# Optimization experiments

Measured on AMD Instinct MI355X. Metric: run time of the kernel, lower is better.

## Reference

```python
import jax, jax.numpy as jnp
import numpy as np

N_NODES = 50000
EPS = 1e-5


def _gcn_edges(edge_index, num_nodes):
    # Add self loops (PyG GCNConv default) and compute symmetric normalization.
    src = jnp.concatenate([edge_index[0], jnp.arange(num_nodes, dtype=edge_index.dtype)])
    dst = jnp.concatenate([edge_index[1], jnp.arange(num_nodes, dtype=edge_index.dtype)])
    deg = jax.ops.segment_sum(jnp.ones_like(dst, dtype=jnp.float32), dst, num_segments=num_nodes)
    dinv = jnp.where(deg > 0, jax.lax.rsqrt(deg), 0.0)
    norm = dinv[src] * dinv[dst]  # [E+N]
    return src, dst, norm


def gcn_conv(x, W, b, src, dst, norm, num_nodes):
    xw = x @ W  # [N, out]
    msg = xw[src] * norm[:, None]  # [E+N, out] gather + scale
    out = jax.ops.segment_sum(msg, dst, num_segments=num_nodes)  # scatter-add
    return out + b


def layer_norm(x, g, b):
    mu = jnp.mean(x, axis=-1, keepdims=True)
    var = jnp.mean(jnp.square(x - mu), axis=-1, keepdims=True)
    return (x - mu) * jax.lax.rsqrt(var + EPS) * g + b


def setup_inputs() -> dict:
    key = jax.random.key(0)
    ks = jax.random.split(key, 12)
    d_in, d_h, d_out = 128, 128, 64
    n_edges = 800000
    x = jax.random.normal(ks[0], (N_NODES, d_in), dtype=jnp.float32)
    edge_index = jax.random.randint(ks[1], (2, n_edges), 0, N_NODES, dtype=jnp.int64)
    s = 1.0 / np.sqrt(d_in)
    return {
        "x": x,
        "edge_index": edge_index,
        "W1": jax.random.uniform(ks[2], (d_in, d_h), jnp.float32, -s, s),
        "b1": jnp.zeros((d_h,), jnp.float32),
        "W2": jax.random.uniform(ks[3], (d_h, d_h), jnp.float32, -s, s),
        "b2": jnp.zeros((d_h,), jnp.float32),
        "W3": jax.random.uniform(ks[4], (d_h, d_out), jnp.float32, -s, s),
        "b3": jnp.zeros((d_out,), jnp.float32),
        "g1": jnp.ones((d_h,), jnp.float32),
        "be1": jnp.zeros((d_h,), jnp.float32),
        "g2": jnp.ones((d_h,), jnp.float32),
        "be2": jnp.zeros((d_h,), jnp.float32),
    }


def reference(x, edge_index, W1, b1, W2, b2, W3, b3, g1, be1, g2, be2):
    num_nodes = x.shape[0]
    src, dst, norm = _gcn_edges(edge_index, num_nodes)
    h = jax.nn.relu(gcn_conv(x, W1, b1, src, dst, norm, num_nodes))
    h = layer_norm(h, g1, be1)  # dropout is identity in eval mode
    h = jax.nn.relu(gcn_conv(h, W2, b2, src, dst, norm, num_nodes))
    h = layer_norm(h, g2, be2)
    return gcn_conv(h, W3, b3, src, dst, norm, num_nodes)
```

## Files before the change

### kernel.cpp

```cpp
#include <hip/hip_runtime.h>

#define EPSV 1e-5f

typedef _Float16 half2_t __attribute__((ext_vector_type(2)));
typedef _Float16 half8_t __attribute__((ext_vector_type(8)));
typedef float float4_t __attribute__((ext_vector_type(4)));

#define BINSH 6
#define BINSZ 64


__global__ __launch_bounds__(256) void k_pre(
    const float* __restrict__ W1, const float* __restrict__ W2,
    const float* __restrict__ W3, _Float16* __restrict__ Wh1,
    _Float16* __restrict__ Wh2, _Float16* __restrict__ Wh3,
    int* __restrict__ cursor, _Float16* __restrict__ ys_y,
    _Float16* __restrict__ ys3, int N, int N1, int zb) {
  int bid = blockIdx.x;
  if (bid < 20) {
    const float* W;
    _Float16* Wh;
    int COLS, t;
    if (bid < 8) { W = W1; Wh = Wh1; COLS = 128; t = bid * 256 + threadIdx.x; }
    else if (bid < 16) { W = W2; Wh = Wh2; COLS = 128; t = (bid - 8) * 256 + threadIdx.x; }
    else { W = W3; Wh = Wh3; COLS = 64; t = (bid - 16) * 256 + threadIdx.x; }
    int NT = (COLS / 16) * 4 * 64;
    if (t >= NT) return;
    int lane = t & 63;
    int ks = (t >> 6) & 3;
    int nb = t >> 8;
    int col = nb * 16 + (lane & 15);
    int k0 = ks * 32 + (lane >> 4) * 8;
    half8_t v;
#pragma unroll
    for (int j = 0; j < 8; j++) v[j] = (_Float16)W[(size_t)(k0 + j) * COLS + col];
    *(half8_t*)&Wh[(size_t)t * 8] = v;
    return;
  }
  if (bid < 20 + zb) {
    int i4 = (bid - 20) * 256 + threadIdx.x;
    if (i4 < ((N + 3) >> 2)) ((int4*)cursor)[i4] = make_int4(0, 0, 0, 0);
    return;
  }
  int t = threadIdx.x;
  half8_t z;
#pragma unroll
  for (int j = 0; j < 8; j++) z[j] = (_Float16)0.f;
  if (t < 16) {
    int s = t >> 2, qq = t & 3;
    *(half8_t*)&ys_y[((size_t)s * N1 + N) * 32 + qq * 8] = z;
  } else if (t < 24) {
    int j = t - 16;
    int s = j >> 2, qq = j & 3;
    *(half8_t*)&ys3[((size_t)s * N1 + N) * 32 + qq * 8] = z;
  }
}


__global__ __launch_bounds__(256) void k_init(
    const int* __restrict__ src, const int* __restrict__ dst,
    int* __restrict__ cursor, int* __restrict__ csr, int E, int N) {
  int b = blockIdx.x;
  int slice = b & 7;
  int lo = (int)(((long long)N * slice) >> 3);
  int hi = (int)(((long long)N * (slice + 1)) >> 3);
  int r = (b >> 3) * 256 + threadIdx.x;
  const int stride = (4096 >> 3) * 256;
  int E4 = E >> 2;
  const int4* dst4 = (const int4*)dst;
  const int4* src4 = (const int4*)src;
  for (int e4 = r; e4 < E4; e4 += stride) {
    int4 d4 = dst4[e4];
    int4 s4 = src4[e4];
    if (d4.x >= lo && d4.x < hi) {
      int pos = atomicAdd(&cursor[d4.x], 1);
      if (pos < BINSZ) csr[((size_t)d4.x << BINSH) + pos] = s4.x;
    }
    if (d4.y >= lo && d4.y < hi) {
      int pos = atomicAdd(&cursor[d4.y], 1);
      if (pos < BINSZ) csr[((size_t)d4.y << BINSH) + pos] = s4.y;
    }
    if (d4.z >= lo && d4.z < hi) {
      int pos = atomicAdd(&cursor[d4.z], 1);
      if (pos < BINSZ) csr[((size_t)d4.z << BINSH) + pos] = s4.z;
    }
    if (d4.w >= lo && d4.w < hi) {
      int pos = atomicAdd(&cursor[d4.w], 1);
      if (pos < BINSZ) csr[((size_t)d4.w << BINSH) + pos] = s4.w;
    }
  }
  if ((E & 3) && (b >> 3) == 0) {
    for (int e = (E & ~3) + threadIdx.x; e < E; e += 256) {
      int d = dst[e];
      if (d >= lo && d < hi) {
        int s = src[e];
        int pos = atomicAdd(&cursor[d], 1);
        if (pos < BINSZ) csr[((size_t)d << BINSH) + pos] = s;
      }
    }
  }
}


template <int COLS, bool LN, typename AT>
__device__ __forceinline__ void gemm_body(
    int bx, const AT* __restrict__ A, const float2* __restrict__ lnp,
    const float* __restrict__ g, const float* __restrict__ be,
    const _Float16* __restrict__ Wh, const int* __restrict__ cursor,
    _Float16* __restrict__ out, int N, int N1) {
  constexpr int NB = COLS / 16;
  int lane = threadIdx.x & 63;
  int w = threadIdx.x >> 6;
  int quad = lane >> 4;
  int mrow = bx * 64 + w * 16 + (lane & 15);
  half8_t af[4];
  if (mrow < N) {
    if constexpr (LN) {
      float P = 0.f, Q = 0.f;
#pragma unroll
      for (int s = 0; s < 4; s++) {
        float2 pq = lnp[(size_t)s * N + mrow];
        P += pq.x; Q += pq.y;
      }
      float mean = P * (1.f / 128.f);
      float rstd = rsqrtf(Q * (1.f / 128.f) - mean * mean + EPSV);
#pragma unroll
      for (int ks = 0; ks < 4; ks++) {
        half8_t sv = *(const half8_t*)&A[((size_t)ks * N1 + mrow) * 32 + quad * 8];
        float4 g0 = *(const float4*)&g[ks * 32 + quad * 8];
        float4 g1 = *(const float4*)&g[ks * 32 + quad * 8 + 4];
        float4 e0 = *(const float4*)&be[ks * 32 + quad * 8];
        float4 e1 = *(const float4*)&be[ks * 32 + quad * 8 + 4];
        af[ks][0] = (_Float16)fmaf(((float)sv[0] - mean) * rstd, g0.x, e0.x);
        af[ks][1] = (_Float16)fmaf(((float)sv[1] - mean) * rstd, g0.y, e0.y);
        af[ks][2] = (_Float16)fmaf(((float)sv[2] - mean) * rstd, g0.z, e0.z);
        af[ks][3] = (_Float16)fmaf(((float)sv[3] - mean) * rstd, g0.w, e0.w);
        af[ks][4] = (_Float16)fmaf(((float)sv[4] - mean) * rstd, g1.x, e1.x);
        af[ks][5] = (_Float16)fmaf(((float)sv[5] - mean) * rstd, g1.y, e1.y);
        af[ks][6] = (_Float16)fmaf(((float)sv[6] - mean) * rstd, g1.z, e1.z);
        af[ks][7] = (_Float16)fmaf(((float)sv[7] - mean) * rstd, g1.w, e1.w);
      }
    } else {
      const AT* ap = A + (size_t)mrow * 128 + quad * 8;
#pragma unroll
      for (int ks = 0; ks < 4; ks++) {
        float4 f0 = *(const float4*)(ap + ks * 32);
        float4 f1 = *(const float4*)(ap + ks * 32 + 4);
        af[ks][0] = (_Float16)f0.x; af[ks][1] = (_Float16)f0.y;
        af[ks][2] = (_Float16)f0.z; af[ks][3] = (_Float16)f0.w;
        af[ks][4] = (_Float16)f1.x; af[ks][5] = (_Float16)f1.y;
        af[ks][6] = (_Float16)f1.z; af[ks][7] = (_Float16)f1.w;
      }
    }
  } else {
#pragma unroll
    for (int ks = 0; ks < 4; ks++)
#pragma unroll
      for (int j = 0; j < 8; j++) af[ks][j] = (_Float16)0.f;
  }
  float4_t acc[NB];
#pragma unroll
  for (int nb = 0; nb < NB; nb++) acc[nb] = (float4_t){0.f, 0.f, 0.f, 0.f};
#pragma unroll
  for (int nb = 0; nb < NB; nb++) {
#pragma unroll
    for (int ks = 0; ks < 4; ks++) {
      half8_t bf = *(const half8_t*)&Wh[(size_t)((nb * 4 + ks) * 64 + lane) * 8];
      acc[nb] = __builtin_amdgcn_mfma_f32_16x16x32_f16(af[ks], bf, acc[nb], 0, 0, 0);
    }
  }
  int orow0 = bx * 64 + w * 16 + quad * 4;
#pragma unroll
  for (int r = 0; r < 4; r++) {
    int row = orow0 + r;
    if (row < N) {
      float dv = rsqrtf((float)(min(cursor[row], BINSZ) + 1));
#pragma unroll
      for (int nb = 0; nb < NB; nb++) {
        int dim = nb * 16 + (lane & 15);
        out[((size_t)(dim >> 5) * N1 + row) * 32 + (dim & 31)] =
            (_Float16)(acc[nb][r] * dv);
      }
    }
  }
}

template <int COLS, bool LN, typename AT>
__global__ __launch_bounds__(256) void k_gemm_mfma(
    const AT* __restrict__ A, const float2* __restrict__ lnp,
    const float* __restrict__ g, const float* __restrict__ be,
    const _Float16* __restrict__ Wh, const int* __restrict__ cursor,
    _Float16* __restrict__ out, int N, int N1) {
  gemm_body<COLS, LN, AT>(blockIdx.x, A, lnp, g, be, Wh, cursor, out, N, N1);
}


__global__ __launch_bounds__(256) void k_aggs(
    const _Float16* __restrict__ ysrc, const int* __restrict__ csr,
    const int* __restrict__ cursor, const float* __restrict__ b,
    _Float16* __restrict__ sdst, float2* __restrict__ lnp, int N, int N1) {
  int slice = blockIdx.x & 3;
  int lane = threadIdx.x & 63;
  int g = lane >> 4, li = lane & 15;
  int q = li & 3, es = li >> 2;
  int node = (blockIdx.x >> 2) * 16 + (threadIdx.x >> 6) * 4 + g;
  const half8_t* yb = (const half8_t*)ysrc + (size_t)slice * N1 * 4;
  int cnt = 0;
  if (node < N) cnt = min(cursor[node], BINSZ);
  int cround = (cnt + 15) & ~15;
  size_t bin = (size_t)node << BINSH;
  float acc[8];
#pragma unroll
  for (int j = 0; j < 8; j++) acc[j] = 0.f;
  const half2_t one2 = {(_Float16)1.f, (_Float16)1.f};
  for (int c = 0; c < cround; c += 16) {
    int idx = N;
    if (c + li < cnt) idx = csr[bin + c + li];
#pragma unroll
    for (int p = 0; p < 2; p++) {
      int sa = __shfl(idx, (g << 4) | (es << 2) | (p << 1), 64);
      int sb = __shfl(idx, (g << 4) | (es << 2) | (p << 1) | 1, 64);
      half8_t ua = yb[(size_t)sa * 4 + q];
      half8_t ub = yb[(size_t)sb * 4 + q];
      const unsigned int* wa = (const unsigned int*)&ua;
      const unsigned int* wb = (const unsigned int*)&ub;
#pragma unroll
      for (int w = 0; w < 4; w++) {
        unsigned int p0 = __builtin_amdgcn_perm(wa[w], wb[w], 0x01000504u);
        unsigned int p1 = __builtin_amdgcn_perm(wa[w], wb[w], 0x03020706u);
        acc[2 * w] = __builtin_amdgcn_fdot2(
            __builtin_bit_cast(half2_t, p0), one2, acc[2 * w], false);
        acc[2 * w + 1] = __builtin_amdgcn_fdot2(
            __builtin_bit_cast(half2_t, p1), one2, acc[2 * w + 1], false);
      }
    }
  }
#pragma unroll
  for (int j = 0; j < 8; j++) {
    acc[j] += __shfl_xor(acc[j], 4, 64);
    acc[j] += __shfl_xor(acc[j], 8, 64);
  }
  half8_t us = yb[(size_t)min(node, N) * 4 + q];
#pragma unroll
  for (int j = 0; j < 8; j++) acc[j] += (float)us[j];
  float di = rsqrtf((float)(cnt + 1));
  float4 b0 = ((const float4*)b)[slice * 8 + q * 2];
  float4 b1 = ((const float4*)b)[slice * 8 + q * 2 + 1];
  float v[8];
  v[0] = fmaxf(fmaf(acc[0], di, b0.x), 0.f);
  v[1] = fmaxf(fmaf(acc[1], di, b0.y), 0.f);
  v[2] = fmaxf(fmaf(acc[2], di, b0.z), 0.f);
  v[3] = fmaxf(fmaf(acc[3], di, b0.w), 0.f);
  v[4] = fmaxf(fmaf(acc[4], di, b1.x), 0.f);
  v[5] = fmaxf(fmaf(acc[5], di, b1.y), 0.f);
  v[6] = fmaxf(fmaf(acc[6], di, b1.z), 0.f);
  v[7] = fmaxf(fmaf(acc[7], di, b1.w), 0.f);
  float p = 0.f, qs = 0.f;
#pragma unroll
  for (int j = 0; j < 8; j++) {
    p += v[j];
    qs = fmaf(v[j], v[j], qs);
  }
  p += __shfl_xor(p, 1, 64);
  p += __shfl_xor(p, 2, 64);
  qs += __shfl_xor(qs, 1, 64);
  qs += __shfl_xor(qs, 2, 64);
  if (node < N) {
    if (li == 0) lnp[(size_t)slice * N + node] = make_float2(p, qs);
    if (es == 0) {
      half8_t o;
#pragma unroll
      for (int j = 0; j < 8; j++) o[j] = (_Float16)v[j];
      ((half8_t*)sdst)[((size_t)slice * N1 + node) * 4 + q] = o;
    }
  }
}


__global__ __launch_bounds__(256) void k_agg_out(
    const _Float16* __restrict__ ysrc, const int* __restrict__ csr,
    const int* __restrict__ cursor, const float* __restrict__ b,
    float* __restrict__ out, int N, int N1) {
  int slice = blockIdx.x & 1;
  int lane = threadIdx.x & 63;
  int g = lane >> 4, li = lane & 15;
  int q = li & 3, es = li >> 2;
  int node = (blockIdx.x >> 1) * 16 + (threadIdx.x >> 6) * 4 + g;
  const half8_t* yb = (const half8_t*)ysrc + (size_t)slice * N1 * 4;
  int cnt = 0;
  if (node < N) cnt = min(cursor[node], BINSZ);
  int cround = (cnt + 15) & ~15;
  size_t bin = (size_t)node << BINSH;
  float acc[8];
#pragma unroll
  for (int j = 0; j < 8; j++) acc[j] = 0.f;
  const half2_t one2 = {(_Float16)1.f, (_Float16)1.f};
  for (int c = 0; c < cround; c += 16) {
    int idx = N;
    if (c + li < cnt) idx = csr[bin + c + li];
#pragma unroll
    for (int p = 0; p < 2; p++) {
      int sa = __shfl(idx, (g << 4) | (es << 2) | (p << 1), 64);
      int sb = __shfl(idx, (g << 4) | (es << 2) | (p << 1) | 1, 64);
      half8_t ua = yb[(size_t)sa * 4 + q];
      half8_t ub = yb[(size_t)sb * 4 + q];
      const unsigned int* wa = (const unsigned int*)&ua;
      const unsigned int* wb = (const unsigned int*)&ub;
#pragma unroll
      for (int w = 0; w < 4; w++) {
        unsigned int p0 = __builtin_amdgcn_perm(wa[w], wb[w], 0x01000504u);
        unsigned int p1 = __builtin_amdgcn_perm(wa[w], wb[w], 0x03020706u);
        acc[2 * w] = __builtin_amdgcn_fdot2(
            __builtin_bit_cast(half2_t, p0), one2, acc[2 * w], false);
        acc[2 * w + 1] = __builtin_amdgcn_fdot2(
            __builtin_bit_cast(half2_t, p1), one2, acc[2 * w + 1], false);
      }
    }
  }
#pragma unroll
  for (int j = 0; j < 8; j++) {
    acc[j] += __shfl_xor(acc[j], 4, 64);
    acc[j] += __shfl_xor(acc[j], 8, 64);
  }
  if (node < N && es == 0) {
    half8_t us = yb[(size_t)node * 4 + q];
#pragma unroll
    for (int j = 0; j < 8; j++) acc[j] += (float)us[j];
    float di = rsqrtf((float)(cnt + 1));
    float4 b0 = ((const float4*)b)[slice * 8 + q * 2];
    float4 b1 = ((const float4*)b)[slice * 8 + q * 2 + 1];
    float4 o0, o1;
    o0.x = fmaf(acc[0], di, b0.x);
    o0.y = fmaf(acc[1], di, b0.y);
    o0.z = fmaf(acc[2], di, b0.z);
    o0.w = fmaf(acc[3], di, b0.w);
    o1.x = fmaf(acc[4], di, b1.x);
    o1.y = fmaf(acc[5], di, b1.y);
    o1.z = fmaf(acc[6], di, b1.z);
    o1.w = fmaf(acc[7], di, b1.w);
    ((float4*)out)[(size_t)node * 16 + slice * 8 + q * 2] = o0;
    ((float4*)out)[(size_t)node * 16 + slice * 8 + q * 2 + 1] = o1;
  }
}


extern "C" void kernel_launch(void* const* d_in, const int* in_sizes, int n_in,
                              void* d_out, int out_size, void* d_ws, size_t ws_size,
                              hipStream_t stream) {
  const float* x = (const float*)d_in[0];
  const int* ei = (const int*)d_in[1];
  const float* W1 = (const float*)d_in[2];
  const float* b1 = (const float*)d_in[3];
  const float* W2 = (const float*)d_in[4];
  const float* b2 = (const float*)d_in[5];
  const float* W3 = (const float*)d_in[6];
  const float* b3 = (const float*)d_in[7];
  const float* g1 = (const float*)d_in[8];
  const float* be1 = (const float*)d_in[9];
  const float* g2 = (const float*)d_in[10];
  const float* be2 = (const float*)d_in[11];

  int N = in_sizes[0] / 128;
  int E = in_sizes[1] / 2;
  int N1 = N + 1;
  const int* srcs = ei;
  const int* dsts = ei + E;

  char* ws = (char*)d_ws;
  size_t off = 0;
  auto alloc = [&](size_t bytes) -> char* {
    char* p = ws + off;
    off = (off + bytes + 255) & ~(size_t)255;
    return p;
  };
  int* cursor = (int*)alloc((size_t)N * 4);
  int* csr = (int*)alloc((size_t)N * BINSZ * 4);
  _Float16* ys_y = (_Float16*)alloc((size_t)4 * N1 * 32 * 2);
  _Float16* ys_s = (_Float16*)alloc((size_t)4 * N1 * 32 * 2);
  _Float16* ys3 = (_Float16*)alloc((size_t)2 * N1 * 32 * 2);
  float2* lnp = (float2*)alloc((size_t)4 * N * 8);
  _Float16* Wh1 = (_Float16*)alloc(128 * 128 * 2);
  _Float16* Wh2 = (_Float16*)alloc(128 * 128 * 2);
  _Float16* Wh3 = (_Float16*)alloc(128 * 64 * 2);

  int gb = (N + 63) / 64;
  int nb16 = (N + 15) / 16;
  int zb = (((N + 3) >> 2) + 255) >> 8;

  k_pre<<<20 + zb + 1, 256, 0, stream>>>(W1, W2, W3, Wh1, Wh2, Wh3,
                                         cursor, ys_y, ys3, N, N1, zb);
  k_init<<<4096, 256, 0, stream>>>(srcs, dsts, cursor, csr, E, N);
  k_gemm_mfma<128, false, float><<<gb, 256, 0, stream>>>(
      x, nullptr, nullptr, nullptr, Wh1, cursor, ys_y, N, N1);
  k_aggs<<<nb16 * 4, 256, 0, stream>>>(ys_y, csr, cursor, b1, ys_s, lnp, N, N1);
  k_gemm_mfma<128, true, _Float16><<<gb, 256, 0, stream>>>(
      ys_s, lnp, g1, be1, Wh2, cursor, ys_y, N, N1);
  k_aggs<<<nb16 * 4, 256, 0, stream>>>(ys_y, csr, cursor, b2, ys_s, lnp, N, N1);
  k_gemm_mfma<64, true, _Float16><<<gb, 256, 0, stream>>>(
      ys_s, lnp, g2, be2, Wh3, cursor, ys3, N, N1);
  k_agg_out<<<nb16 * 2, 256, 0, stream>>>(ys3, csr, cursor, b3,
                                          (float*)d_out, N, N1);
}
```

Measured before the change: 244.2 us.

## Fuse first GEMM with CSR fill and apply source degree scaling in aggregation

The first layer's GEMM no longer needs degree counts, so it is merged into the CSR-building kernel as extra blocks and runs concurrently with the atomic binning. Because the GEMM output is now unscaled, the first aggregation kernel applies the per-source rsqrt-degree weight inside the fdot2 and scales the self term by the node's own factor. The cursor array grows by one entry and is zeroed so the padding node index N reads a valid count. This removes one kernel launch and its serialization, at the cost of extra cursor gathers per edge in the first aggregation and fp16 rounding of the weights.

Result: no change. 247.3 us (+1.3%).

```diff
diff --git a/kernel.cpp b/kernel.cpp
--- a/kernel.cpp
+++ b/kernel.cpp
@@ -39,7 +39,7 @@
   }
   if (bid < 20 + zb) {
     int i4 = (bid - 20) * 256 + threadIdx.x;
-    if (i4 < ((N + 3) >> 2)) ((int4*)cursor)[i4] = make_int4(0, 0, 0, 0);
+    if (i4 < ((N1 + 3) >> 2)) ((int4*)cursor)[i4] = make_int4(0, 0, 0, 0);
     return;
   }
   int t = threadIdx.x;
@@ -57,10 +57,111 @@
 }
 
 
-__global__ __launch_bounds__(256) void k_init(
+template <int COLS, bool LN, bool SCALE, typename AT>
+__device__ __forceinline__ void gemm_body(
+    int bx, const AT* __restrict__ A, const float2* __restrict__ lnp,
+    const float* __restrict__ g, const float* __restrict__ be,
+    const _Float16* __restrict__ Wh, const int* __restrict__ cursor,
+    _Float16* __restrict__ out, int N, int N1) {
+  constexpr int NB = COLS / 16;
+  int lane = threadIdx.x & 63;
+  int w = threadIdx.x >> 6;
+  int quad = lane >> 4;
+  int mrow = bx * 64 + w * 16 + (lane & 15);
+  half8_t af[4];
+  if (mrow < N) {
+    if constexpr (LN) {
+      float P = 0.f, Q = 0.f;
+#pragma unroll
+      for (int s = 0; s < 4; s++) {
+        float2 pq = lnp[(size_t)s * N + mrow];
+        P += pq.x; Q += pq.y;
+      }
+      float mean = P * (1.f / 128.f);
+      float rstd = rsqrtf(Q * (1.f / 128.f) - mean * mean + EPSV);
+#pragma unroll
+      for (int ks = 0; ks < 4; ks++) {
+        half8_t sv = *(const half8_t*)&A[((size_t)ks * N1 + mrow) * 32 + quad * 8];
+        float4 g0 = *(const float4*)&g[ks * 32 + quad * 8];
+        float4 g1 = *(const float4*)&g[ks * 32 + quad * 8 + 4];
+        float4 e0 = *(const float4*)&be[ks * 32 + quad * 8];
+        float4 e1 = *(const float4*)&be[ks * 32 + quad * 8 + 4];
+        af[ks][0] = (_Float16)fmaf(((float)sv[0] - mean) * rstd, g0.x, e0.x);
+        af[ks][1] = (_Float16)fmaf(((float)sv[1] - mean) * rstd, g0.y, e0.y);
+        af[ks][2] = (_Float16)fmaf(((float)sv[2] - mean) * rstd, g0.z, e0.z);
+        af[ks][3] = (_Float16)fmaf(((float)sv[3] - mean) * rstd, g0.w, e0.w);
+        af[ks][4] = (_Float16)fmaf(((float)sv[4] - mean) * rstd, g1.x, e1.x);
+        af[ks][5] = (_Float16)fmaf(((float)sv[5] - mean) * rstd, g1.y, e1.y);
+        af[ks][6] = (_Float16)fmaf(((float)sv[6] - mean) * rstd, g1.z, e1.z);
+        af[ks][7] = (_Float16)fmaf(((float)sv[7] - mean) * rstd, g1.w, e1.w);
+      }
+    } else {
+      const AT* ap = A + (size_t)mrow * 128 + quad * 8;
+#pragma unroll
+      for (int ks = 0; ks < 4; ks++) {
+        float4 f0 = *(const float4*)(ap + ks * 32);
+        float4 f1 = *(const float4*)(ap + ks * 32 + 4);
+        af[ks][0] = (_Float16)f0.x; af[ks][1] = (_Float16)f0.y;
+        af[ks][2] = (_Float16)f0.z; af[ks][3] = (_Float16)f0.w;
+        af[ks][4] = (_Float16)f1.x; af[ks][5] = (_Float16)f1.y;
+        af[ks][6] = (_Float16)f1.z; af[ks][7] = (_Float16)f1.w;
+      }
+    }
+  } else {
+#pragma unroll
+    for (int ks = 0; ks < 4; ks++)
+#pragma unroll
+      for (int j = 0; j < 8; j++) af[ks][j] = (_Float16)0.f;
+  }
+  float4_t acc[NB];
+#pragma unroll
+  for (int nb = 0; nb < NB; nb++) acc[nb] = (float4_t){0.f, 0.f, 0.f, 0.f};
+#pragma unroll
+  for (int nb = 0; nb < NB; nb++) {
+#pragma unroll
+    for (int ks = 0; ks < 4; ks++) {
+      half8_t bf = *(const half8_t*)&Wh[(size_t)((nb * 4 + ks) * 64 + lane) * 8];
+      acc[nb] = __builtin_amdgcn_mfma_f32_16x16x32_f16(af[ks], bf, acc[nb], 0, 0, 0);
+    }
+  }
+  int orow0 = bx * 64 + w * 16 + quad * 4;
+#pragma unroll
+  for (int r = 0; r < 4; r++) {
+    int row = orow0 + r;
+    if (row < N) {
+      float dv = 1.f;
+      if constexpr (SCALE) dv = rsqrtf((float)(min(cursor[row], BINSZ) + 1));
+#pragma unroll
+      for (int nb = 0; nb < NB; nb++) {
+        int dim = nb * 16 + (lane & 15);
+        out[((size_t)(dim >> 5) * N1 + row) * 32 + (dim & 31)] =
+            (_Float16)(SCALE ? acc[nb][r] * dv : acc[nb][r]);
+      }
+    }
+  }
+}
+
+template <int COLS, bool LN, bool SCALE, typename AT>
+__global__ __launch_bounds__(256) void k_gemm_mfma(
+    const AT* __restrict__ A, const float2* __restrict__ lnp,
+    const float* __restrict__ g, const float* __restrict__ be,
+    const _Float16* __restrict__ Wh, const int* __restrict__ cursor,
+    _Float16* __restrict__ out, int N, int N1) {
+  gemm_body<COLS, LN, SCALE, AT>(blockIdx.x, A, lnp, g, be, Wh, cursor, out, N, N1);
+}
+
+
+__global__ __launch_bounds__(256) void k_fill_gemm1(
+    const float* __restrict__ x, const _Float16* __restrict__ Wh1,
     const int* __restrict__ src, const int* __restrict__ dst,
-    int* __restrict__ cursor, int* __restrict__ csr, int E, int N) {
-  int b = blockIdx.x;
+    int* __restrict__ cursor, int* __restrict__ csr,
+    _Float16* __restrict__ ys_y, int E, int N, int N1, int gb) {
+  if ((int)blockIdx.x < gb) {
+    gemm_body<128, false, false, float>(blockIdx.x, x, nullptr, nullptr,
+                                        nullptr, Wh1, nullptr, ys_y, N, N1);
+    return;
+  }
+  int b = blockIdx.x - gb;
   int slice = b & 7;
   int lo = (int)(((long long)N * slice) >> 3);
   int hi = (int)(((long long)N * (slice + 1)) >> 3);
@@ -102,99 +203,7 @@
 }
 
 
-template <int COLS, bool LN, typename AT>
-__device__ __forceinline__ void gemm_body(
-    int bx, const AT* __restrict__ A, const float2* __restrict__ lnp,
-    const float* __restrict__ g, const float* __restrict__ be,
-    const _Float16* __restrict__ Wh, const int* __restrict__ cursor,
-    _Float16* __restrict__ out, int N, int N1) {
-  constexpr int NB = COLS / 16;
-  int lane = threadIdx.x & 63;
-  int w = threadIdx.x >> 6;
-  int quad = lane >> 4;
-  int mrow = bx * 64 + w * 16 + (lane & 15);
-  half8_t af[4];
-  if (mrow < N) {
-    if constexpr (LN) {
-      float P = 0.f, Q = 0.f;
-#pragma unroll
-      for (int s = 0; s < 4; s++) {
-        float2 pq = lnp[(size_t)s * N + mrow];
-        P += pq.x; Q += pq.y;
-      }
-      float mean = P * (1.f / 128.f);
-      float rstd = rsqrtf(Q * (1.f / 128.f) - mean * mean + EPSV);
-#pragma unroll
-      for (int ks = 0; ks < 4; ks++) {
-        half8_t sv = *(const half8_t*)&A[((size_t)ks * N1 + mrow) * 32 + quad * 8];
-        float4 g0 = *(const float4*)&g[ks * 32 + quad * 8];
-        float4 g1 = *(const float4*)&g[ks * 32 + quad * 8 + 4];
-        float4 e0 = *(const float4*)&be[ks * 32 + quad * 8];
-        float4 e1 = *(const float4*)&be[ks * 32 + quad * 8 + 4];
-        af[ks][0] = (_Float16)fmaf(((float)sv[0] - mean) * rstd, g0.x, e0.x);
-        af[ks][1] = (_Float16)fmaf(((float)sv[1] - mean) * rstd, g0.y, e0.y);
-        af[ks][2] = (_Float16)fmaf(((float)sv[2] - mean) * rstd, g0.z, e0.z);
-        af[ks][3] = (_Float16)fmaf(((float)sv[3] - mean) * rstd, g0.w, e0.w);
-        af[ks][4] = (_Float16)fmaf(((float)sv[4] - mean) * rstd, g1.x, e1.x);
-        af[ks][5] = (_Float16)fmaf(((float)sv[5] - mean) * rstd, g1.y, e1.y);
-        af[ks][6] = (_Float16)fmaf(((float)sv[6] - mean) * rstd, g1.z, e1.z);
-        af[ks][7] = (_Float16)fmaf(((float)sv[7] - mean) * rstd, g1.w, e1.w);
-      }
-    } else {
-      const AT* ap = A + (size_t)mrow * 128 + quad * 8;
-#pragma unroll
-      for (int ks = 0; ks < 4; ks++) {
-        float4 f0 = *(const float4*)(ap + ks * 32);
-        float4 f1 = *(const float4*)(ap + ks * 32 + 4);
-        af[ks][0] = (_Float16)f0.x; af[ks][1] = (_Float16)f0.y;
-        af[ks][2] = (_Float16)f0.z; af[ks][3] = (_Float16)f0.w;
-        af[ks][4] = (_Float16)f1.x; af[ks][5] = (_Float16)f1.y;
-        af[ks][6] = (_Float16)f1.z; af[ks][7] = (_Float16)f1.w;
-      }
-    }
-  } else {
-#pragma unroll
-    for (int ks = 0; ks < 4; ks++)
-#pragma unroll
-      for (int j = 0; j < 8; j++) af[ks][j] = (_Float16)0.f;
-  }
-  float4_t acc[NB];
-#pragma unroll
-  for (int nb = 0; nb < NB; nb++) acc[nb] = (float4_t){0.f, 0.f, 0.f, 0.f};
-#pragma unroll
-  for (int nb = 0; nb < NB; nb++) {
-#pragma unroll
-    for (int ks = 0; ks < 4; ks++) {
-      half8_t bf = *(const half8_t*)&Wh[(size_t)((nb * 4 + ks) * 64 + lane) * 8];
-      acc[nb] = __builtin_amdgcn_mfma_f32_16x16x32_f16(af[ks], bf, acc[nb], 0, 0, 0);
-    }
-  }
-  int orow0 = bx * 64 + w * 16 + quad * 4;
-#pragma unroll
-  for (int r = 0; r < 4; r++) {
-    int row = orow0 + r;
-    if (row < N) {
-      float dv = rsqrtf((float)(min(cursor[row], BINSZ) + 1));
-#pragma unroll
-      for (int nb = 0; nb < NB; nb++) {
-        int dim = nb * 16 + (lane & 15);
-        out[((size_t)(dim >> 5) * N1 + row) * 32 + (dim & 31)] =
-            (_Float16)(acc[nb][r] * dv);
-      }
-    }
-  }
-}
-
-template <int COLS, bool LN, typename AT>
-__global__ __launch_bounds__(256) void k_gemm_mfma(
-    const AT* __restrict__ A, const float2* __restrict__ lnp,
-    const float* __restrict__ g, const float* __restrict__ be,
-    const _Float16* __restrict__ Wh, const int* __restrict__ cursor,
-    _Float16* __restrict__ out, int N, int N1) {
-  gemm_body<COLS, LN, AT>(blockIdx.x, A, lnp, g, be, Wh, cursor, out, N, N1);
-}
-
-
+template <bool EW>
 __global__ __launch_bounds__(256) void k_aggs(
     const _Float16* __restrict__ ysrc, const int* __restrict__ csr,
     const int* __restrict__ cursor, const float* __restrict__ b,
@@ -222,6 +231,15 @@
       int sb = __shfl(idx, (g << 4) | (es << 2) | (p << 1) | 1, 64);
       half8_t ua = yb[(size_t)sa * 4 + q];
       half8_t ub = yb[(size_t)sb * 4 + q];
+      half2_t dw;
+      if constexpr (EW) {
+        float fa = rsqrtf((float)(min(cursor[sa], BINSZ) + 1));
+        float fb = rsqrtf((float)(min(cursor[sb], BINSZ) + 1));
+        dw[0] = (_Float16)fa;
+        dw[1] = (_Float16)fb;
+      } else {
+        dw = one2;
+      }
       const unsigned int* wa = (const unsigned int*)&ua;
       const unsigned int* wb = (const unsigned int*)&ub;
 #pragma unroll
@@ -229,9 +247,9 @@
         unsigned int p0 = __builtin_amdgcn_perm(wa[w], wb[w], 0x01000504u);
         unsigned int p1 = __builtin_amdgcn_perm(wa[w], wb[w], 0x03020706u);
         acc[2 * w] = __builtin_amdgcn_fdot2(
-            __builtin_bit_cast(half2_t, p0), one2, acc[2 * w], false);
+            __builtin_bit_cast(half2_t, p0), dw, acc[2 * w], false);
         acc[2 * w + 1] = __builtin_amdgcn_fdot2(
-            __builtin_bit_cast(half2_t, p1), one2, acc[2 * w + 1], false);
+            __builtin_bit_cast(half2_t, p1), dw, acc[2 * w + 1], false);
       }
     }
   }
@@ -240,10 +258,13 @@
     acc[j] += __shfl_xor(acc[j], 4, 64);
     acc[j] += __shfl_xor(acc[j], 8, 64);
   }
+  float di = rsqrtf((float)(cnt + 1));
   half8_t us = yb[(size_t)min(node, N) * 4 + q];
 #pragma unroll
-  for (int j = 0; j < 8; j++) acc[j] += (float)us[j];
-  float di = rsqrtf((float)(cnt + 1));
+  for (int j = 0; j < 8; j++) {
+    if constexpr (EW) acc[j] = fmaf((float)us[j], di, acc[j]);
+    else acc[j] += (float)us[j];
+  }
   float4 b0 = ((const float4*)b)[slice * 8 + q * 2];
   float4 b1 = ((const float4*)b)[slice * 8 + q * 2 + 1];
   float v[8];
@@ -373,7 +394,7 @@
     off = (off + bytes + 255) & ~(size_t)255;
     return p;
   };
-  int* cursor = (int*)alloc((size_t)N * 4);
+  int* cursor = (int*)alloc((size_t)N1 * 4 + 16);
   int* csr = (int*)alloc((size_t)N * BINSZ * 4);
   _Float16* ys_y = (_Float16*)alloc((size_t)4 * N1 * 32 * 2);
   _Float16* ys_s = (_Float16*)alloc((size_t)4 * N1 * 32 * 2);
@@ -385,18 +406,19 @@
 
   int gb = (N + 63) / 64;
   int nb16 = (N + 15) / 16;
-  int zb = (((N + 3) >> 2) + 255) >> 8;
+  int zb = (((N1 + 3) >> 2) + 255) >> 8;
 
   k_pre<<<20 + zb + 1, 256, 0, stream>>>(W1, W2, W3, Wh1, Wh2, Wh3,
                                          cursor, ys_y, ys3, N, N1, zb);
-  k_init<<<4096, 256, 0, stream>>>(srcs, dsts, cursor, csr, E, N);
-  k_gemm_mfma<128, false, float><<<gb, 256, 0, stream>>>(
-      x, nullptr, nullptr, nullptr, Wh1, cursor, ys_y, N, N1);
-  k_aggs<<<nb16 * 4, 256, 0, stream>>>(ys_y, csr, cursor, b1, ys_s, lnp, N, N1);
-  k_gemm_mfma<128, true, _Float16><<<gb, 256, 0, stream>>>(
+  k_fill_gemm1<<<gb + 4096, 256, 0, stream>>>(x, Wh1, srcs, dsts, cursor, csr,
+                                              ys_y, E, N, N1, gb);
+  k_aggs<true><<<nb16 * 4, 256, 0, stream>>>(ys_y, csr, cursor, b1, ys_s, lnp,
+                                             N, N1);
+  k_gemm_mfma<128, true, true, _Float16><<<gb, 256, 0, stream>>>(
       ys_s, lnp, g1, be1, Wh2, cursor, ys_y, N, N1);
-  k_aggs<<<nb16 * 4, 256, 0, stream>>>(ys_y, csr, cursor, b2, ys_s, lnp, N, N1);
-  k_gemm_mfma<64, true, _Float16><<<gb, 256, 0, stream>>>(
+  k_aggs<false><<<nb16 * 4, 256, 0, stream>>>(ys_y, csr, cursor, b2, ys_s, lnp,
+                                              N, N1);
+  k_gemm_mfma<64, true, true, _Float16><<<gb, 256, 0, stream>>>(
       ys_s, lnp, g2, be2, Wh3, cursor, ys3, N, N1);
   k_agg_out<<<nb16 * 2, 256, 0, stream>>>(ys3, csr, cursor, b3,
                                           (float*)d_out, N, N1);
```
